# Kernel tuning notes

Hardware: AMD Instinct MI355X
Metric: run time of the kernel (lower is better)

## Reference

```python
import jax, jax.numpy as jnp
import numpy as np

S = (256, 256, 256)          # MRI volume shape
N = 50000                    # number of Gaussians
T = 16                       # fixed tile edge; covers max bbox width = 2*3*sigma_max*(S-1)+2 <= 15
SIG_MIN, SIG_MAX = 0.004, 0.008  # NN-distance-based sigma range (k_sigma=1)


def setup_inputs() -> dict:
    key = jax.random.key(0)
    k1, k2, k3 = jax.random.split(key, 3)
    centers = jax.random.uniform(k1, (N, 3), dtype=jnp.float32)
    sigmas = jax.random.uniform(k2, (N,), dtype=jnp.float32, minval=SIG_MIN, maxval=SIG_MAX)
    intensities = jax.random.uniform(k3, (N,), dtype=jnp.float32)
    return {"centers": centers, "sigmas": sigmas, "intensities": intensities}


def _splat(centers, sigmas, intensities):
    dt = centers.dtype
    scale = jnp.asarray([s - 1 for s in S], dtype=dt)            # (3,) == scale_factors
    shape_f = jnp.asarray(S, dtype=dt)                           # (3,)
    shape_i = jnp.asarray(S, dtype=jnp.int32)                    # (3,)

    center_vox = centers * scale                                 # (N,3) voxel-space centers
    cutoff = 3.0 * sigmas[:, None] * scale                       # (N,3)
    # original: min_idx = max(c-cut, 0).int(); max_idx = (min(c+cut, scale)+1).int(), clipped to S
    min_idx = jnp.floor(jnp.maximum(center_vox - cutoff, 0.0)).astype(jnp.int32)          # (N,3)
    max_idx = jnp.minimum(jnp.floor(jnp.minimum(center_vox + cutoff, scale)) + 1.0,
                          shape_f).astype(jnp.int32)             # (N,3), exclusive

    ar = jnp.arange(T, dtype=jnp.int32)
    idx = min_idx[:, :, None] + ar[None, None, :]                # (N,3,T) absolute voxel idx
    valid = idx < max_idx[:, :, None]                            # (N,3,T) inside variable bbox
    idx_c = jnp.minimum(idx, shape_i[None, :, None] - 1)         # clamp for safe gather/scatter

    # grid coordinate along axis a at voxel i is i/(S_a-1) (linspace(0,1,S_a))
    coord = idx_c.astype(dt) / scale[None, :, None]              # (N,3,T)
    d = coord - centers[:, :, None]                              # (N,3,T)
    d2 = (d[:, 0, :, None, None] ** 2
          + d[:, 1, None, :, None] ** 2
          + d[:, 2, None, None, :] ** 2)                         # (N,T,T,T)
    mask = (valid[:, 0, :, None, None]
            & valid[:, 1, None, :, None]
            & valid[:, 2, None, None, :])                        # (N,T,T,T)

    inv_two_sig2 = 0.5 / (sigmas * sigmas)                       # (N,)
    contrib = intensities[:, None, None, None] * jnp.exp(-d2 * inv_two_sig2[:, None, None, None])
    contrib = jnp.where(mask, contrib, jnp.zeros((), dt))        # (N,T,T,T)

    lin = (idx_c[:, 0, :, None, None] * (S[1] * S[2])
           + idx_c[:, 1, None, :, None] * S[2]
           + idx_c[:, 2, None, None, :])                         # (N,T,T,T) flat voxel index

    vol = jnp.zeros(S[0] * S[1] * S[2], dtype=dt)
    vol = vol.at[lin.reshape(-1)].add(contrib.reshape(-1))
    return vol.reshape(S)


def reference(centers, sigmas, intensities):
    return _splat(centers, sigmas, intensities)
```

## Files before the change

kernel.cpp:

```cpp
#include <hip/hip_runtime.h>


#define NT3    4096
#define CAP    128
#define INV255 (1.0f/255.0f)

__global__ __launch_bounds__(256) void bin_prep_kernel(
    const float* __restrict__ centers,
    const float* __restrict__ sigmas,
    const float* __restrict__ intens,
    int*    __restrict__ counts,
    float4* __restrict__ prep,
    int2*   __restrict__ list,
    int N)
{
    int g = blockIdx.x * 256 + threadIdx.x;
    if (g >= N) return;
    float c0 = centers[3*g+0], c1 = centers[3*g+1], c2 = centers[3*g+2];
    float sig = sigmas[g];
    float cut = 3.0f * sig * 255.0f;
    float c[3] = {c0, c1, c2};
    int mn[3], mx[3];
    #pragma unroll
    for (int a = 0; a < 3; ++a) {
        float cv = c[a] * 255.0f;
        mn[a] = (int)floorf(fmaxf(cv - cut, 0.0f));
        mx[a] = (int)fminf(floorf(fminf(cv + cut, 255.0f)) + 1.0f, 256.0f);
    }
    prep[2*g+0] = make_float4(c0, c1, c2, 0.5f / (sig * sig));
    prep[2*g+1] = make_float4(intens[g], 0.0f, 0.0f, 0.0f);

    int t0x = mn[0] >> 4, t1x = (mx[0] - 1) >> 4;
    int t0y = mn[1] >> 4, t1y = (mx[1] - 1) >> 4;
    int t0z = mn[2] >> 4, t1z = (mx[2] - 1) >> 4;
    for (int tx = t0x; tx <= t1x; ++tx) {
        int lox = max(mn[0] - (tx << 4), 0), hix = min(mx[0] - (tx << 4), 16);
        for (int ty = t0y; ty <= t1y; ++ty) {
            int loy = max(mn[1] - (ty << 4), 0), hiy = min(mx[1] - (ty << 4), 16);
            for (int tz = t0z; tz <= t1z; ++tz) {
                int loz = max(mn[2] - (tz << 4), 0), hiz = min(mx[2] - (tz << 4), 16);
                unsigned cl = (unsigned)lox | ((unsigned)hix << 5)
                            | ((unsigned)loy << 10) | ((unsigned)hiy << 15)
                            | ((unsigned)loz << 20) | ((unsigned)hiz << 25);
                int t = (tx << 8) | (ty << 4) | tz;
                int slot = atomicAdd(&counts[t], 1);
                if (slot < CAP) list[t * CAP + slot] = make_int2(g, (int)cl);
            }
        }
    }
}

__global__ __launch_bounds__(256) void splat_main(
    const float4* __restrict__ prep,
    const int*    __restrict__ counts,
    const int2*   __restrict__ list,
    float* __restrict__ vol)
{
    int b  = blockIdx.x;
    int ox = (b >> 8) << 4, oy = ((b >> 4) & 15) << 4, oz = (b & 15) << 4;
    int n  = counts[b]; if (n > CAP) n = CAP;
    int base = b * CAP;
    int tid  = threadIdx.x;
    int ly   = tid >> 4, lz = tid & 15;
    int tap  = tid & 15;

    float fy = (float)(oy + ly) * INV255;
    float fz = (float)(oz + lz) * INV255;
    float fx = (float)(ox + tap) * INV255;

    float acc[16];
    #pragma unroll
    for (int i = 0; i < 16; ++i) acc[i] = 0.0f;

    for (int k = 0; k < n; ++k) {
        int2 e = list[base + k];
        int g = e.x;
        unsigned cl = (unsigned)e.y;
        int lox = cl & 31,          hix = (cl >> 5) & 31;
        int loy = (cl >> 10) & 31,  hiy = (cl >> 15) & 31;
        int loz = (cl >> 20) & 31,  hiz = (cl >> 25) & 31;
        float4 p0 = prep[2*g+0];
        float4 p1 = prep[2*g+1];

        float dy = fy - p0.y, dz = fz - p0.z;
        float d2 = fmaf(dy, dy, dz * dz);
        bool vyz = (ly >= loy) & (ly < hiy) & (lz >= loz) & (lz < hiz);
        float eyz = vyz ? __expf(-d2 * p0.w) * p1.x : 0.0f;
        if (__ballot(eyz != 0.0f) == 0ULL) continue;

        float dx = fx - p0.x;
        bool vx = (tap >= lox) & (tap < hix);
        float ex = vx ? __expf(-dx * dx * p0.w) : 0.0f;
        int exb = __float_as_int(ex);

        if (hix <= 8) {
            #pragma unroll
            for (int i = 0; i < 8; ++i) {
                float sx = __int_as_float(__builtin_amdgcn_readlane(exb, i));
                acc[i] = fmaf(sx, eyz, acc[i]);
            }
        } else if (lox >= 8) {
            #pragma unroll
            for (int i = 8; i < 16; ++i) {
                float sx = __int_as_float(__builtin_amdgcn_readlane(exb, i));
                acc[i] = fmaf(sx, eyz, acc[i]);
            }
        } else {
            #pragma unroll
            for (int i = 0; i < 16; ++i) {
                float sx = __int_as_float(__builtin_amdgcn_readlane(exb, i));
                acc[i] = fmaf(sx, eyz, acc[i]);
            }
        }
    }

    int ybase = ((oy + ly) << 8) + (oz + lz);
    #pragma unroll
    for (int i = 0; i < 16; ++i)
        vol[((ox + i) << 16) + ybase] = acc[i];
}

extern "C" void kernel_launch(void* const* d_in, const int* in_sizes, int n_in,
                              void* d_out, int out_size, void* d_ws, size_t ws_size,
                              hipStream_t stream) {
    const float* centers = (const float*)d_in[0];
    const float* sigmas  = (const float*)d_in[1];
    const float* intens  = (const float*)d_in[2];
    float* vol = (float*)d_out;
    const int N = in_sizes[1];

    char* ws = (char*)d_ws;
    int*    counts = (int*)ws;
    float4* prep   = (float4*)(ws + 16 * 1024);
    int2*   list   = (int2*)(ws + 16 * 1024 + (size_t)N * 32);

    hipMemsetAsync(counts, 0, NT3 * sizeof(int), stream);

    int gblocks = (N + 255) / 256;
    bin_prep_kernel<<<gblocks, 256, 0, stream>>>(centers, sigmas, intens,
                                                 counts, prep, list, N);
    splat_main<<<NT3, 256, 0, stream>>>(prep, counts, list, vol);
}
```

Baseline: 150.6 us.

## Shrink tiles to 8^3 with one wavefront per tile and scalar list reads

Switches from 16^3 tiles, each handled by a 256-thread block, to 8^3 tiles, each handled by one 64-lane wavefront, so a block now covers four tiles. The per-tile clip bounds are no longer stored in the bin list; they are recomputed from packed min/max indices kept in the prep record. Exponentials move to exp2 with a precomputed log2e-scaled weight in voxel units. The idea is to cut wasted lanes and long per-tile lists from the large tiles. In exchange, Gaussians straddle more tiles, which means more atomics and duplicate list entries, the ballot early-exit is dropped, and the lower per-tile cap of 64 raises the risk of overflow.

```diff
diff --git a/kernel.cpp b/kernel.cpp
--- a/kernel.cpp
+++ b/kernel.cpp
@@ -1,9 +1,9 @@
 #include <hip/hip_runtime.h>
 
 
-#define NT3    4096
-#define CAP    128
-#define INV255 (1.0f/255.0f)
+#define NTILE  32768
+#define CAP    64
+#define LOG2E  1.4426950408889634f
 
 __global__ __launch_bounds__(256) void bin_prep_kernel(
     const float* __restrict__ centers,
@@ -11,7 +11,7 @@
     const float* __restrict__ intens,
     int*    __restrict__ counts,
     float4* __restrict__ prep,
-    int2*   __restrict__ list,
+    int*    __restrict__ list,
     int N)
 {
     int g = blockIdx.x * 256 + threadIdx.x;
@@ -27,96 +27,81 @@
         mn[a] = (int)floorf(fmaxf(cv - cut, 0.0f));
         mx[a] = (int)fminf(floorf(fminf(cv + cut, 255.0f)) + 1.0f, 256.0f);
     }
-    prep[2*g+0] = make_float4(c0, c1, c2, 0.5f / (sig * sig));
-    prep[2*g+1] = make_float4(intens[g], 0.0f, 0.0f, 0.0f);
+    float s255 = sig * 255.0f;
+    float w2 = -0.5f * LOG2E / (s255 * s255);
+    unsigned mnp = (unsigned)mn[0] | ((unsigned)mn[1] << 10) | ((unsigned)mn[2] << 20);
+    unsigned mxp = (unsigned)mx[0] | ((unsigned)mx[1] << 10) | ((unsigned)mx[2] << 20);
+    prep[2*g+0] = make_float4(c0 * 255.0f, c1 * 255.0f, c2 * 255.0f, w2);
+    prep[2*g+1] = make_float4(intens[g], __uint_as_float(mnp), __uint_as_float(mxp), 0.0f);
 
-    int t0x = mn[0] >> 4, t1x = (mx[0] - 1) >> 4;
-    int t0y = mn[1] >> 4, t1y = (mx[1] - 1) >> 4;
-    int t0z = mn[2] >> 4, t1z = (mx[2] - 1) >> 4;
-    for (int tx = t0x; tx <= t1x; ++tx) {
-        int lox = max(mn[0] - (tx << 4), 0), hix = min(mx[0] - (tx << 4), 16);
-        for (int ty = t0y; ty <= t1y; ++ty) {
-            int loy = max(mn[1] - (ty << 4), 0), hiy = min(mx[1] - (ty << 4), 16);
+    int t0x = mn[0] >> 3, t1x = (mx[0] - 1) >> 3;
+    int t0y = mn[1] >> 3, t1y = (mx[1] - 1) >> 3;
+    int t0z = mn[2] >> 3, t1z = (mx[2] - 1) >> 3;
+    for (int tx = t0x; tx <= t1x; ++tx)
+        for (int ty = t0y; ty <= t1y; ++ty)
             for (int tz = t0z; tz <= t1z; ++tz) {
-                int loz = max(mn[2] - (tz << 4), 0), hiz = min(mx[2] - (tz << 4), 16);
-                unsigned cl = (unsigned)lox | ((unsigned)hix << 5)
-                            | ((unsigned)loy << 10) | ((unsigned)hiy << 15)
-                            | ((unsigned)loz << 20) | ((unsigned)hiz << 25);
-                int t = (tx << 8) | (ty << 4) | tz;
+                int t = (tx << 10) | (ty << 5) | tz;
                 int slot = atomicAdd(&counts[t], 1);
-                if (slot < CAP) list[t * CAP + slot] = make_int2(g, (int)cl);
+                if (slot < CAP) list[t * CAP + slot] = g;
             }
-        }
-    }
 }
 
 __global__ __launch_bounds__(256) void splat_main(
     const float4* __restrict__ prep,
     const int*    __restrict__ counts,
-    const int2*   __restrict__ list,
+    const int*    __restrict__ list,
     float* __restrict__ vol)
 {
-    int b  = blockIdx.x;
-    int ox = (b >> 8) << 4, oy = ((b >> 4) & 15) << 4, oz = (b & 15) << 4;
-    int n  = counts[b]; if (n > CAP) n = CAP;
-    int base = b * CAP;
-    int tid  = threadIdx.x;
-    int ly   = tid >> 4, lz = tid & 15;
-    int tap  = tid & 15;
+    int wid = threadIdx.x >> 6;
+    int t   = __builtin_amdgcn_readfirstlane(blockIdx.x * 4 + wid);
+    int tx = t >> 10, ty = (t >> 5) & 31, tz = t & 31;
+    int ox = tx << 3, oy = ty << 3, oz = tz << 3;
+    int lane = threadIdx.x & 63;
+    int ly = lane >> 3, lz = lane & 7, tap = lane & 7;
 
-    float fy = (float)(oy + ly) * INV255;
-    float fz = (float)(oz + lz) * INV255;
-    float fx = (float)(ox + tap) * INV255;
+    int n    = counts[t]; if (n > CAP) n = CAP;
+    int base = t * CAP;
 
-    float acc[16];
+    float fyv = (float)(oy + ly);
+    float fzv = (float)(oz + lz);
+    float fxv = (float)(ox + tap);
+
+    float acc[8];
     #pragma unroll
-    for (int i = 0; i < 16; ++i) acc[i] = 0.0f;
+    for (int i = 0; i < 8; ++i) acc[i] = 0.0f;
 
     for (int k = 0; k < n; ++k) {
-        int2 e = list[base + k];
-        int g = e.x;
-        unsigned cl = (unsigned)e.y;
-        int lox = cl & 31,          hix = (cl >> 5) & 31;
-        int loy = (cl >> 10) & 31,  hiy = (cl >> 15) & 31;
-        int loz = (cl >> 20) & 31,  hiz = (cl >> 25) & 31;
+        int g = __builtin_amdgcn_readfirstlane(list[base + k]);
         float4 p0 = prep[2*g+0];
         float4 p1 = prep[2*g+1];
 
-        float dy = fy - p0.y, dz = fz - p0.z;
-        float d2 = fmaf(dy, dy, dz * dz);
+        unsigned mnp = __float_as_uint(p1.y);
+        unsigned mxp = __float_as_uint(p1.z);
+        int lox = max((int)( mnp        & 1023) - ox, 0), hix = min((int)( mxp        & 1023) - ox, 8);
+        int loy = max((int)((mnp >> 10) & 1023) - oy, 0), hiy = min((int)((mxp >> 10) & 1023) - oy, 8);
+        int loz = max((int)((mnp >> 20) & 1023) - oz, 0), hiz = min((int)((mxp >> 20) & 1023) - oz, 8);
+
+        float dy = fyv - p0.y, dz = fzv - p0.z;
+        float eyz = exp2f(fmaf(dy, dy, dz * dz) * p0.w) * p1.x;
         bool vyz = (ly >= loy) & (ly < hiy) & (lz >= loz) & (lz < hiz);
-        float eyz = vyz ? __expf(-d2 * p0.w) * p1.x : 0.0f;
-        if (__ballot(eyz != 0.0f) == 0ULL) continue;
+        eyz = vyz ? eyz : 0.0f;
 
-        float dx = fx - p0.x;
+        float dx = fxv - p0.x;
+        float exv = exp2f(dx * dx * p0.w);
         bool vx = (tap >= lox) & (tap < hix);
-        float ex = vx ? __expf(-dx * dx * p0.w) : 0.0f;
-        int exb = __float_as_int(ex);
+        exv = vx ? exv : 0.0f;
+        int exb = __float_as_int(exv);
 
-        if (hix <= 8) {
-            #pragma unroll
-            for (int i = 0; i < 8; ++i) {
-                float sx = __int_as_float(__builtin_amdgcn_readlane(exb, i));
-                acc[i] = fmaf(sx, eyz, acc[i]);
-            }
-        } else if (lox >= 8) {
-            #pragma unroll
-            for (int i = 8; i < 16; ++i) {
-                float sx = __int_as_float(__builtin_amdgcn_readlane(exb, i));
-                acc[i] = fmaf(sx, eyz, acc[i]);
-            }
-        } else {
-            #pragma unroll
-            for (int i = 0; i < 16; ++i) {
-                float sx = __int_as_float(__builtin_amdgcn_readlane(exb, i));
-                acc[i] = fmaf(sx, eyz, acc[i]);
-            }
+        #pragma unroll
+        for (int i = 0; i < 8; ++i) {
+            float sx = __int_as_float(__builtin_amdgcn_readlane(exb, i));
+            acc[i] = fmaf(sx, eyz, acc[i]);
         }
     }
 
     int ybase = ((oy + ly) << 8) + (oz + lz);
     #pragma unroll
-    for (int i = 0; i < 16; ++i)
+    for (int i = 0; i < 8; ++i)
         vol[((ox + i) << 16) + ybase] = acc[i];
 }
 
@@ -131,13 +116,13 @@
 
     char* ws = (char*)d_ws;
     int*    counts = (int*)ws;
-    float4* prep   = (float4*)(ws + 16 * 1024);
-    int2*   list   = (int2*)(ws + 16 * 1024 + (size_t)N * 32);
+    float4* prep   = (float4*)(ws + (size_t)NTILE * sizeof(int));
+    int*    list   = (int*)(ws + (size_t)NTILE * sizeof(int) + (size_t)N * 32);
 
-    hipMemsetAsync(counts, 0, NT3 * sizeof(int), stream);
+    hipMemsetAsync(counts, 0, NTILE * sizeof(int), stream);
 
     int gblocks = (N + 255) / 256;
     bin_prep_kernel<<<gblocks, 256, 0, stream>>>(centers, sigmas, intens,
                                                  counts, prep, list, N);
-    splat_main<<<NT3, 256, 0, stream>>>(prep, counts, list, vol);
+    splat_main<<<NTILE / 4, 256, 0, stream>>>(prep, counts, list, vol);
 }
```

Result: faster. 144.2 us (-4.2%).
